# Kernel optimization log

Hardware: AMD Instinct MI355X
Metric: run time of the kernel (lower is better)

The kernel has to match this reference:

```python
import jax, jax.numpy as jnp
import numpy as np

B, D, L = 8, 512, 4096
NHEAD = 8
HEAD_DIM = D // NHEAD
TRUNC_STD = 0.02


def setup_inputs() -> dict:
    key = jax.random.key(0)
    ks = jax.random.split(key, 7)
    return {
        "x": jax.random.normal(ks[0], (B, D, L, 1), jnp.float32),
        "y": jax.random.normal(ks[1], (B, D, 1, 1), jnp.float32),
        "Wq": jax.random.normal(ks[2], (D, D), jnp.float32) * TRUNC_STD,
        "Wk": jax.random.normal(ks[3], (D, D), jnp.float32) * TRUNC_STD,
        "Wv": jax.random.normal(ks[4], (D, D), jnp.float32) * TRUNC_STD,
        "WO_ring": jax.random.normal(ks[5], (D, D), jnp.float32) * TRUNC_STD,
        "bO_ring": jnp.zeros((D,), jnp.float32),
        "WO_star": jax.random.normal(ks[6], (D, D), jnp.float32) * TRUNC_STD,
        "bO_star": jnp.zeros((D,), jnp.float32),
    }


def reference(x, y, Wq, Wk, Wv, WO_ring, bO_ring, WO_star, bO_star):
    Bx, Dx, Lx, _ = x.shape
    hd = Dx // NHEAD
    scale = 1.0 / np.sqrt(hd).astype(np.float32)

    # concat relay token on the sequence axis, project q/k/v over channels
    xy = jnp.concatenate([x, y], axis=2)[..., 0]            # [B, D, L+1]
    xy = jnp.transpose(xy, (0, 2, 1))                       # [B, L+1, D]
    q = jnp.transpose(xy @ Wq, (0, 2, 1))                   # [B, D, L+1]
    k = jnp.transpose(xy @ Wk, (0, 2, 1))
    v = jnp.transpose(xy @ Wv, (0, 2, 1))

    # ---- ring (local window-3 + relay) attention over the L node tokens ----
    qn = q[:, :, :Lx].reshape(Bx, NHEAD, hd, Lx)            # [B,n,h,L]
    kn, vn = k[:, :, :Lx], v[:, :, :Lx]                     # [B,D,L]
    kr, vr = k[:, :, Lx], v[:, :, Lx]                       # [B,D]

    def window3(t):
        # extract_patches SAME with size 3: slot w holds t[:, :, l-1+w], zero-padded
        tp = jnp.pad(t, ((0, 0), (0, 0), (1, 1)))
        tw = jnp.stack([tp[:, :, w:w + Lx] for w in range(3)], axis=2)  # [B,D,3,L]
        return tw.reshape(Bx, NHEAD, hd, 3, Lx)

    kr_b = jnp.broadcast_to(kr.reshape(Bx, NHEAD, hd, 1, 1), (Bx, NHEAD, hd, 1, Lx))
    vr_b = jnp.broadcast_to(vr.reshape(Bx, NHEAD, hd, 1, 1), (Bx, NHEAD, hd, 1, Lx))
    kw = jnp.concatenate([window3(kn), kr_b], axis=3)       # [B,n,h,4,L]
    vw = jnp.concatenate([window3(vn), vr_b], axis=3)

    scores = jnp.einsum('bnhl,bnhwl->bnwl', qn, kw) * scale  # [B,n,4,L]
    alphas = jax.nn.softmax(scores, axis=2)                  # softmax over window
    att = jnp.einsum('bnwl,bnhwl->bnhl', alphas, vw).reshape(Bx, Dx, Lx)
    nodes = jnp.einsum('bdl,de->bel', att, WO_ring) + bO_ring[None, :, None]
    nodes = nodes[..., None]                                 # [B, D, L, 1]

    # ---- star (relay) attention: relay query attends to all L+1 tokens ----
    qr = q[:, :, Lx].reshape(Bx, NHEAD, 1, hd)              # [B,n,1,h]
    ka = k.reshape(Bx, NHEAD, hd, Lx + 1)                   # [B,n,h,L+1]
    va = v.reshape(Bx, NHEAD, hd, Lx + 1)
    s = jnp.einsum('bnoh,bnhl->bnol', qr, ka) * scale       # [B,n,1,L+1]
    a = jax.nn.softmax(s, axis=-1)
    att_r = jnp.einsum('bnol,bnhl->bnoh', a, va).reshape(Bx, Dx)
    relay = (att_r @ WO_star + bO_star).reshape(Bx, Dx, 1, 1)

    return nodes, relay
```

## Files before the change

kernel.cpp:

```cpp
#include <hip/hip_runtime.h>

#define BB 8
#define DD 512
#define LL 4096
#define NH 8
#define HD 64
#define SCALE 0.125f
#define NCH 16
#define CH 256

typedef __attribute__((ext_vector_type(8))) short short8;
typedef __attribute__((ext_vector_type(4))) float f32x4;

static __device__ __forceinline__ float bf2f(unsigned short u) {
  union { float f; unsigned int i; } c; c.i = ((unsigned int)u) << 16; return c.f;
}
static __device__ __forceinline__ unsigned short f2bf(float f) {
  union { float f; unsigned int i; } c; c.f = f;
  unsigned int i = c.i;
  unsigned int r = (i + 0x7fffu + ((i >> 16) & 1u)) >> 16;
  return (unsigned short)r;
}

static __device__ __forceinline__ void gload_lds16(const void* g, void* l) {
  __builtin_amdgcn_global_load_lds(
      (const __attribute__((address_space(1))) void*)g,
      (__attribute__((address_space(3))) void*)l, 16, 0, 0);
}

static __device__ __forceinline__ float waveSum(float v) {
#pragma unroll
  for (int o = 32; o; o >>= 1) v += __shfl_down(v, o, 64);
  return v;
}
static __device__ __forceinline__ float waveMax(float v) {
#pragma unroll
  for (int o = 32; o; o >>= 1) v = fmaxf(v, __shfl_down(v, o, 64));
  return v;
}
static __device__ __forceinline__ float grp8Sum(float v) {
  v += __shfl_xor(v, 1, 8);
  v += __shfl_xor(v, 2, 8);
  v += __shfl_xor(v, 4, 8);
  return v;
}
static __device__ float blockSum(float v, float* red) {
  const int lane = threadIdx.x & 63, wid = threadIdx.x >> 6;
  const int nw = (int)(blockDim.x >> 6);
  v = waveSum(v);
  if (lane == 0) red[wid] = v;
  __syncthreads();
  if (wid == 0) {
    float t = (lane < nw) ? red[lane] : 0.f;
    t = waveSum(t);
    if (lane == 0) red[0] = t;
  }
  __syncthreads();
  float r = red[0];
  __syncthreads();
  return r;
}
static __device__ float blockMax(float v, float* red) {
  const int lane = threadIdx.x & 63, wid = threadIdx.x >> 6;
  const int nw = (int)(blockDim.x >> 6);
  v = waveMax(v);
  if (lane == 0) red[wid] = v;
  __syncthreads();
  if (wid == 0) {
    float t = (lane < nw) ? red[lane] : -1e30f;
    t = waveMax(t);
    if (lane == 0) red[0] = t;
  }
  __syncthreads();
  float r = red[0];
  __syncthreads();
  return r;
}

__global__ __launch_bounds__(256) void prep_w4(
    const float* __restrict__ w0, const float* __restrict__ w1,
    const float* __restrict__ w2, const float* __restrict__ w3,
    unsigned short* __restrict__ o0, unsigned short* __restrict__ o1,
    unsigned short* __restrict__ o2, unsigned short* __restrict__ o3) {
  const int s = blockIdx.z;
  const float* win = (s == 0) ? w0 : (s == 1) ? w1 : (s == 2) ? w2 : w3;
  unsigned short* wout = (s == 0) ? o0 : (s == 1) ? o1 : (s == 2) ? o2 : o3;
  const int d0 = blockIdx.y * 64;
  const int m0 = blockIdx.x * 64;
  __shared__ float t[64][65];
  const int tid = threadIdx.x;
  const int r = tid >> 4;
  const int c4 = (tid & 15) * 4;
#pragma unroll
  for (int p = 0; p < 4; p++) {
    const float4 v = *(const float4*)(win + (size_t)(d0 + p * 16 + r) * DD + m0 + c4);
    *(float4*)&t[p * 16 + r][c4] = v;
  }
  __syncthreads();
#pragma unroll
  for (int p = 0; p < 4; p++) {
    const int ll = p * 16 + r;
    ushort4 o;
    o.x = f2bf(t[c4 + 0][ll]);
    o.y = f2bf(t[c4 + 1][ll]);
    o.z = f2bf(t[c4 + 2][ll]);
    o.w = f2bf(t[c4 + 3][ll]);
    *(ushort4*)(wout + (size_t)(m0 + ll) * DD + d0 + c4) = o;
  }
}

__global__ __launch_bounds__(256) void prep_x(
    const float* __restrict__ x, unsigned short* __restrict__ xt) {
  const int b = blockIdx.z;
  const int e0 = blockIdx.y * 64;
  const int l0 = blockIdx.x * 64;
  __shared__ float t[64][65];
  const int tid = threadIdx.x;
  const int r = tid >> 4;
  const int c4 = (tid & 15) * 4;
  const float* xb = x + (size_t)b * DD * LL;
#pragma unroll
  for (int p = 0; p < 4; p++) {
    const float4 v = *(const float4*)(xb + (size_t)(e0 + p * 16 + r) * LL + l0 + c4);
    *(float4*)&t[p * 16 + r][c4] = v;
  }
  __syncthreads();
#pragma unroll
  for (int p = 0; p < 4; p++) {
    const int ll = p * 16 + r;
    ushort4 o;
    o.x = f2bf(t[c4 + 0][ll]);
    o.y = f2bf(t[c4 + 1][ll]);
    o.z = f2bf(t[c4 + 2][ll]);
    o.w = f2bf(t[c4 + 3][ll]);
    *(ushort4*)(xt + ((size_t)b * LL + l0 + ll) * DD + e0 + c4) = o;
  }
}

#define STAGEH(g, s)                                       \
  do {                                                     \
    gload_lds16((g) + sgoff, (s) + sloff);                 \
    gload_lds16((g) + sgoff + 32, (s) + sloff + 4096);     \
  } while (0)

#define READ_A(dst, base, ib)                                           \
  _Pragma("unroll") for (int i = 0; i < 4; i++) {                       \
    dst[i][0] = *(const short8*)((base) + ((ib) + i) * 512);            \
    dst[i][1] = *(const short8*)((base) + ((ib) + i) * 512 + 4096);     \
  }

#define READ_B(base, qn_)                                               \
  _Pragma("unroll") for (int j = 0; j < 2; j++) {                       \
    bb[j][0] = *(const short8*)((base) + (qn_) * 1024 + j * 512);       \
    bb[j][1] = *(const short8*)((base) + (qn_) * 1024 + j * 512 + 4096);\
  }

#define MFMA16(AF, IO, JO)                                                    \
  __builtin_amdgcn_s_setprio(1);                                              \
  _Pragma("unroll") for (int i = 0; i < 4; i++)                               \
  _Pragma("unroll") for (int j = 0; j < 2; j++) {                             \
    acc[(IO) + i][(JO) + j] = __builtin_amdgcn_mfma_f32_16x16x32_bf16(        \
        AF[i][0], bb[j][0], acc[(IO) + i][(JO) + j], 0, 0, 0);                \
    acc[(IO) + i][(JO) + j] = __builtin_amdgcn_mfma_f32_16x16x32_bf16(        \
        AF[i][1], bb[j][1], acc[(IO) + i][(JO) + j], 0, 0, 0);                \
  }                                                                           \
  __builtin_amdgcn_s_setprio(0);

#define PHASE_SYNC_PRE                                     \
  __builtin_amdgcn_s_barrier();                            \
  asm volatile("s_waitcnt lgkmcnt(0)" ::: "memory");       \
  __builtin_amdgcn_sched_barrier(0);

#define PHASE_SYNC_POST                                    \
  __builtin_amdgcn_sched_barrier(0);                       \
  __builtin_amdgcn_s_barrier();

__global__ __launch_bounds__(512, 2) void qkv_mfma_8ph(
    const unsigned short* __restrict__ Wt, const unsigned short* __restrict__ Xt,
    unsigned short* __restrict__ qn, unsigned short* __restrict__ kn,
    unsigned short* __restrict__ vn) {
  extern __shared__ __align__(16) unsigned short sm[];
  const int b = blockIdx.z;
  const int m0 = blockIdx.y * 256;
  const int n0 = blockIdx.x * 256;
  const int tid = threadIdx.x;
  const int lane = tid & 63, w = tid >> 6;
  const int wm = w >> 2, wn = w & 3;
  const int l15 = lane & 15, lh = lane >> 4;

  const unsigned short* Ag = Wt + (size_t)m0 * DD;
  const unsigned short* Bg = Xt + ((size_t)b * LL + n0) * DD;

  const int kswz = (lh << 3) ^ ((l15 & 8) << 1);
  const unsigned short* aB = sm + wm * 8192 + l15 * 32 + kswz;
  const unsigned short* bB = sm + 32768 + (wn >> 1) * 8192 + (wn & 1) * 2048 +
                             l15 * 32 + kswz;

  const int srow = (w << 4) + (lane >> 2);
  const size_t sgoff = (size_t)srow * DD + ((size_t)(((lane & 3) << 3) ^ ((srow & 8) << 1)));
  const int sloff = w * 512;

  f32x4 acc[8][4];
#pragma unroll
  for (int i = 0; i < 8; i++)
#pragma unroll
    for (int j = 0; j < 4; j++) acc[i][j] = (f32x4){0.f, 0.f, 0.f, 0.f};

  STAGEH(Ag, sm);
  STAGEH(Ag + 128 * DD, sm + 8192);
  STAGEH(Bg, sm + 32768);
  STAGEH(Bg + 128 * DD, sm + 32768 + 8192);
  STAGEH(Ag + 64, sm + 16384);
  STAGEH(Ag + 128 * DD + 64, sm + 16384 + 8192);
  asm volatile("s_waitcnt vmcnt(4)" ::: "memory");
  __builtin_amdgcn_s_barrier();

  short8 a0[4][2], a1[4][2], bb[2][2];
  for (int u = 0; u < 8; ++u) {
    const int slot = u & 1;
    const unsigned short* aS = aB + slot * 16384;
    const unsigned short* bS = bB + slot * 16384;
    const unsigned short* An = Ag + (u + 2) * 64;
    const unsigned short* Bn = Bg + (u + 1) * 64;
    unsigned short* sAd = sm + slot * 16384;
    unsigned short* sBd = sm + 32768 + (slot ^ 1) * 16384;

    READ_A(a0, aS, 0);
    READ_B(bS, 0);
    if (u < 7) STAGEH(Bn, sBd);
    PHASE_SYNC_PRE
    MFMA16(a0, 0, 0)
    PHASE_SYNC_POST
    READ_A(a1, aS, 4);
    if (u < 7) STAGEH(Bn + 128 * DD, sBd + 8192);
    PHASE_SYNC_PRE
    MFMA16(a1, 4, 0)
    PHASE_SYNC_POST
    READ_B(bS, 1);
    if (u < 6) STAGEH(An, sAd);
    PHASE_SYNC_PRE
    MFMA16(a0, 0, 2)
    PHASE_SYNC_POST
    if (u < 6) STAGEH(An + 128 * DD, sAd + 8192);
    __builtin_amdgcn_s_barrier();
    asm volatile("s_waitcnt lgkmcnt(0)" ::: "memory");
    __builtin_amdgcn_sched_barrier(0);
    MFMA16(a1, 4, 2)
    __builtin_amdgcn_sched_barrier(0);
    if (u < 6) {
      asm volatile("s_waitcnt vmcnt(4)" ::: "memory");
    } else if (u == 6) {
      asm volatile("s_waitcnt vmcnt(0)" ::: "memory");
    }
    __builtin_amdgcn_s_barrier();
  }

  __syncthreads();
#pragma unroll
  for (int i = 0; i < 8; i++)
#pragma unroll
    for (int j = 0; j < 4; j++) {
      const int dloc = wm * 128 + i * 16 + lh * 4;
      const int lloc = wn * 64 + j * 16 + l15;
      ushort4 pk;
      pk.x = f2bf(acc[i][j][0]);
      pk.y = f2bf(acc[i][j][1]);
      pk.z = f2bf(acc[i][j][2]);
      pk.w = f2bf(acc[i][j][3]);
      *(ushort4*)((char*)sm + ((lloc * 512 + dloc * 2) ^ ((lloc & 7) << 4))) = pk;
    }
  __syncthreads();
  const int sector = m0 >> 9;
  unsigned short* outp = ((sector == 0) ? qn : (sector == 1) ? kn : vn) +
                         (size_t)b * LL * DD + (m0 & 511);
#pragma unroll
  for (int it = 0; it < 16; it++) {
    const int flat = it * 8192 + tid * 16;
    const int lloc = flat >> 9;
    const int off = flat & 511;
    const short8 vdat =
        *(const short8*)((const char*)sm + lloc * 512 + (off ^ ((lloc & 7) << 4)));
    *(short8*)(outp + (size_t)(n0 + lloc) * DD + (off >> 1)) = vdat;
  }
}

__global__ __launch_bounds__(256) void nodes_mfma(
    const unsigned short* __restrict__ Wt, const unsigned short* __restrict__ At,
    const float* __restrict__ bo, float* __restrict__ out) {
  const int wgid = blockIdx.x + 32 * (blockIdx.y + 4 * blockIdx.z);
  const int swz = (wgid & 7) * 128 + (wgid >> 3);
  const int b = swz >> 7;
  const int rem = swz & 127;
  const int n0 = (rem >> 2) * 128;
  const int m0 = (rem & 3) * 128;
  __shared__ short As[128 * 32];
  __shared__ short Bs[128 * 32];
  const int tid = threadIdx.x;
  const int lane = tid & 63, w = tid >> 6;
  const int wm = w & 1, wn = w >> 1;

  const unsigned short* Ag = Wt + (size_t)m0 * DD;
  const unsigned short* Bg = At + ((size_t)b * LL + n0) * DD;
  const int srow = lane >> 2;
  const int scol = (lane & 3) * 8;

  f32x4 acc[4][4];
#pragma unroll
  for (int i = 0; i < 4; i++)
#pragma unroll
    for (int j = 0; j < 4; j++) acc[i][j] = (f32x4){0.f, 0.f, 0.f, 0.f};

  for (int k0 = 0; k0 < DD; k0 += 32) {
    __syncthreads();
#pragma unroll
    for (int p = 0; p < 2; p++) {
      const int c = w * 2 + p;
      gload_lds16(Ag + (size_t)(c * 16 + srow) * DD + k0 + scol, (short*)As + c * 16 * 32);
      gload_lds16(Bg + (size_t)(c * 16 + srow) * DD + k0 + scol, (short*)Bs + c * 16 * 32);
    }
    __syncthreads();
    short8 af[4], bfr[4];
#pragma unroll
    for (int i = 0; i < 4; i++)
      af[i] = *(const short8*)&As[(wm * 64 + i * 16 + (lane & 15)) * 32 + (lane >> 4) * 8];
#pragma unroll
    for (int j = 0; j < 4; j++)
      bfr[j] = *(const short8*)&Bs[(wn * 64 + j * 16 + (lane & 15)) * 32 + (lane >> 4) * 8];
#pragma unroll
    for (int i = 0; i < 4; i++)
#pragma unroll
      for (int j = 0; j < 4; j++)
        acc[i][j] = __builtin_amdgcn_mfma_f32_16x16x32_bf16(af[i], bfr[j], acc[i][j], 0, 0, 0);
  }

  float* outp = out + (size_t)b * DD * LL;
  const int ebase = m0 + wm * 64;
  const int col0 = n0 + wn * 64 + (lane & 15);
#pragma unroll
  for (int i = 0; i < 4; i++) {
    const int e0 = ebase + i * 16 + (lane >> 4) * 4;
#pragma unroll
    for (int j = 0; j < 4; j++) {
      const int cc = col0 + j * 16;
#pragma unroll
      for (int r = 0; r < 4; r++)
        outp[(size_t)(e0 + r) * LL + cc] = acc[i][j][r] + bo[e0 + r];
    }
  }
}

__global__ __launch_bounds__(256) void relay_qkv(
    const float* __restrict__ y, const float* __restrict__ Wq,
    const float* __restrict__ Wk, const float* __restrict__ Wv,
    float* __restrict__ qr, float* __restrict__ kr, float* __restrict__ vr) {
  const int b = blockIdx.y;
  const int d = blockIdx.x * 256 + threadIdx.x;
  __shared__ float ys[DD];
  for (int i = threadIdx.x; i < DD; i += 256) ys[i] = y[b * DD + i];
  __syncthreads();
  float aq = 0.f, ak = 0.f, av = 0.f;
  for (int e = 0; e < DD; e++) {
    const float yv = ys[e];
    aq = fmaf(yv, Wq[(size_t)e * DD + d], aq);
    ak = fmaf(yv, Wk[(size_t)e * DD + d], ak);
    av = fmaf(yv, Wv[(size_t)e * DD + d], av);
  }
  qr[b * DD + d] = aq;
  kr[b * DD + d] = ak;
  vr[b * DD + d] = av;
}

__global__ __launch_bounds__(256) void local_attn(
    const unsigned short* __restrict__ qn, const unsigned short* __restrict__ kn,
    const unsigned short* __restrict__ vn, const float* __restrict__ kr,
    const float* __restrict__ vr, unsigned short* __restrict__ att_t) {
  const int b = blockIdx.z, n = blockIdx.y;
  const int tid = threadIdx.x;
  const int li = tid >> 3, dl = tid & 7;
  const int l0 = blockIdx.x * 32;
  const int l = l0 + li;
  __shared__ float krs[HD], vrs[HD];
  __shared__ __align__(16) char ksb[34 * 128];
  __shared__ __align__(16) char vsb[34 * 128];
  const int rb = b * DD + n * HD;
  if (tid < HD) { krs[tid] = kr[rb + tid]; vrs[tid] = vr[rb + tid]; }

  {
    const int s1 = tid >> 3;
    const int gl1 = min(max(l0 - 1 + s1, 0), LL - 1);
    const size_t gb1 = ((size_t)b * LL + gl1) * DD + n * HD + dl * 8;
    const int so1 = s1 * 128 + dl * 16;
    *(short8*)(ksb + so1) = *(const short8*)(kn + gb1);
    *(short8*)(vsb + so1) = *(const short8*)(vn + gb1);
    if (tid < 16) {
      const int s2 = 32 + (tid >> 3);
      const int gl2 = min(l0 - 1 + s2, LL - 1);
      const size_t gb2 = ((size_t)b * LL + gl2) * DD + n * HD + dl * 8;
      const int so2 = s2 * 128 + dl * 16;
      *(short8*)(ksb + so2) = *(const short8*)(kn + gb2);
      *(short8*)(vsb + so2) = *(const short8*)(vn + gb2);
    }
  }
  __syncthreads();

  const size_t rowbase = ((size_t)b * LL + l) * DD + n * HD + dl * 8;
  const bool has_m = (l > 0), has_p = (l < LL - 1);
  const int lo = dl * 16;

  const short8 q8 = *(const short8*)(qn + rowbase);
  const short8 km8 = *(const short8*)(ksb + (li + 0) * 128 + lo);
  const short8 k08 = *(const short8*)(ksb + (li + 1) * 128 + lo);
  const short8 kp8 = *(const short8*)(ksb + (li + 2) * 128 + lo);

  float s0 = 0.f, s1 = 0.f, s2 = 0.f, s3 = 0.f;
  float qf[8];
#pragma unroll
  for (int j = 0; j < 8; j++) {
    qf[j] = bf2f((unsigned short)q8[j]);
    s0 = fmaf(qf[j], bf2f((unsigned short)km8[j]), s0);
    s1 = fmaf(qf[j], bf2f((unsigned short)k08[j]), s1);
    s2 = fmaf(qf[j], bf2f((unsigned short)kp8[j]), s2);
    s3 = fmaf(qf[j], krs[dl * 8 + j], s3);
  }
  s0 = grp8Sum(s0) * SCALE;
  s1 = grp8Sum(s1) * SCALE;
  s2 = grp8Sum(s2) * SCALE;
  s3 = grp8Sum(s3) * SCALE;
  if (!has_m) s0 = 0.f;
  if (!has_p) s2 = 0.f;
  const float m = fmaxf(fmaxf(s0, s1), fmaxf(s2, s3));
  const float e0 = __expf(s0 - m), e1 = __expf(s1 - m);
  const float e2 = __expf(s2 - m), e3 = __expf(s3 - m);
  const float inv = 1.f / (e0 + e1 + e2 + e3);
  const float a0 = has_m ? e0 * inv : 0.f;
  const float a1 = e1 * inv;
  const float a2 = has_p ? e2 * inv : 0.f;
  const float a3 = e3 * inv;

  const short8 vm8 = *(const short8*)(vsb + (li + 0) * 128 + lo);
  const short8 v08 = *(const short8*)(vsb + (li + 1) * 128 + lo);
  const short8 vp8 = *(const short8*)(vsb + (li + 2) * 128 + lo);
  short8 o8;
#pragma unroll
  for (int j = 0; j < 8; j++) {
    float o = a0 * bf2f((unsigned short)vm8[j]) + a1 * bf2f((unsigned short)v08[j]) +
              a2 * bf2f((unsigned short)vp8[j]) + a3 * vrs[dl * 8 + j];
    o8[j] = (short)f2bf(o);
  }
  *(short8*)(att_t + rowbase) = o8;
}

__global__ __launch_bounds__(256) void relay_attn_part(
    const float* __restrict__ qr, const unsigned short* __restrict__ kn,
    const unsigned short* __restrict__ vn, float* __restrict__ part) {
  const int ch = blockIdx.x, n = blockIdx.y, b = blockIdx.z;
  const int tid = threadIdx.x;
  const int li = tid >> 3, dl = tid & 7;
  __shared__ float qs[HD];
  __shared__ float sv[CH];
  __shared__ float red[17];
  __shared__ float os[32][68];
  const int rb = b * DD + n * HD;
  if (tid < HD) qs[tid] = qr[rb + tid];
  __syncthreads();
  const size_t base = ((size_t)b * LL + ch * CH) * DD + n * HD + dl * 8;

#pragma unroll
  for (int it = 0; it < 8; it++) {
    const int lr2 = it * 32 + li;
    const short8 kc = *(const short8*)(kn + base + (size_t)lr2 * DD);
    float p = 0.f;
#pragma unroll
    for (int j = 0; j < 8; j++) p = fmaf(qs[dl * 8 + j], bf2f((unsigned short)kc[j]), p);
    p = grp8Sum(p);
    if (dl == 0) sv[lr2] = p * SCALE;
  }
  __syncthreads();
  const float s = sv[tid];
  const float m = blockMax(s, red);
  const float pp = __expf(s - m);
  sv[tid] = pp;
  const float sum = blockSum(pp, red);

  float oc[8];
#pragma unroll
  for (int j = 0; j < 8; j++) oc[j] = 0.f;
#pragma unroll
  for (int it = 0; it < 8; it++) {
    const int lr2 = it * 32 + li;
    const float p = sv[lr2];
    const short8 vc = *(const short8*)(vn + base + (size_t)lr2 * DD);
#pragma unroll
    for (int j = 0; j < 8; j++) oc[j] = fmaf(p, bf2f((unsigned short)vc[j]), oc[j]);
  }
#pragma unroll
  for (int j = 0; j < 8; j++) os[li][dl * 8 + j] = oc[j];
  __syncthreads();
  float* po = part + (((size_t)b * NH + n) * NCH + ch) * 68;
  if (tid < HD) {
    float t = 0.f;
#pragma unroll 8
    for (int g = 0; g < 32; g++) t += os[g][tid];
    po[tid] = t;
  }
  if (tid == 64) { po[64] = m; po[65] = sum; }
}

__global__ __launch_bounds__(64) void relay_attn_combine(
    const float* __restrict__ qr, const float* __restrict__ krr,
    const float* __restrict__ vrr, const float* __restrict__ part,
    float* __restrict__ attr) {
  const int n = blockIdx.x, b = blockIdx.y;
  const int h = threadIdx.x;
  const int rb = b * DD + n * HD;
  float t = qr[rb + h] * krr[rb + h];
  t = waveSum(t);
  const float s_r = __shfl(t, 0, 64) * SCALE;
  const float* po = part + (((size_t)b * NH + n) * NCH) * 68;
  float M = s_r;
#pragma unroll
  for (int c = 0; c < NCH; c++) M = fmaxf(M, po[c * 68 + 64]);
  float S = __expf(s_r - M);
  float o = S * vrr[rb + h];
#pragma unroll
  for (int c = 0; c < NCH; c++) {
    const float e = __expf(po[c * 68 + 64] - M);
    S = fmaf(po[c * 68 + 65], e, S);
    o = fmaf(po[c * 68 + h], e, o);
  }
  attr[rb + h] = o / S;
}

__global__ __launch_bounds__(256) void relay_proj(
    const float* __restrict__ attr, const float* __restrict__ Wstar,
    const float* __restrict__ bstar, float* __restrict__ out) {
  const int b = blockIdx.y;
  const int e = blockIdx.x * 256 + threadIdx.x;
  __shared__ float as[DD];
  for (int i = threadIdx.x; i < DD; i += 256) as[i] = attr[b * DD + i];
  __syncthreads();
  float acc = bstar[e];
  for (int d = 0; d < DD; d++) acc = fmaf(as[d], Wstar[(size_t)d * DD + e], acc);
  out[(size_t)BB * DD * LL + b * DD + e] = acc;
}

extern "C" void kernel_launch(void* const* d_in, const int* in_sizes, int n_in,
                              void* d_out, int out_size, void* d_ws, size_t ws_size,
                              hipStream_t stream) {
  const float* x   = (const float*)d_in[0];
  const float* y   = (const float*)d_in[1];
  const float* Wq  = (const float*)d_in[2];
  const float* Wk  = (const float*)d_in[3];
  const float* Wv  = (const float*)d_in[4];
  const float* WOr = (const float*)d_in[5];
  const float* bOr = (const float*)d_in[6];
  const float* WOs = (const float*)d_in[7];
  const float* bOs = (const float*)d_in[8];
  float* out = (float*)d_out;

  char* ws = (char*)d_ws;
  const size_t SZ = (size_t)BB * DD * LL * sizeof(unsigned short);
  unsigned short* qn  = (unsigned short*)(ws);
  unsigned short* kn  = (unsigned short*)(ws + SZ);
  unsigned short* vn  = (unsigned short*)(ws + 2 * SZ);
  unsigned short* xt  = (unsigned short*)(ws + 3 * SZ);
  unsigned short* att_t = xt;
  unsigned short* Wallt = (unsigned short*)(ws + 4 * SZ);
  unsigned short* WOrt  = (unsigned short*)(ws + 4 * SZ + 1536 * 512 * 2);
  float* qr   = (float*)(ws + 4 * SZ + 2048 * 512 * 2);
  float* kr   = qr + BB * DD;
  float* vr   = kr + BB * DD;
  float* attr = vr + BB * DD;
  float* part = attr + BB * DD;

  static int smaxset = 0;
  if (!smaxset) {
    (void)hipFuncSetAttribute((const void*)qkv_mfma_8ph,
                              hipFuncAttributeMaxDynamicSharedMemorySize, 131072);
    smaxset = 1;
  }

  prep_w4<<<dim3(8, 8, 4), 256, 0, stream>>>(
      Wq, Wk, Wv, WOr,
      Wallt, Wallt + (size_t)512 * 512, Wallt + (size_t)1024 * 512, WOrt);
  prep_x<<<dim3(64, 8, BB), 256, 0, stream>>>(x, xt);

  qkv_mfma_8ph<<<dim3(16, 6, BB), 512, 131072, stream>>>(Wallt, xt, qn, kn, vn);
  relay_qkv<<<dim3(DD / 256, BB), 256, 0, stream>>>(y, Wq, Wk, Wv, qr, kr, vr);
  local_attn<<<dim3(LL / 32, NH, BB), 256, 0, stream>>>(qn, kn, vn, kr, vr, att_t);
  nodes_mfma<<<dim3(32, 4, BB), 256, 0, stream>>>(WOrt, att_t, bOr, out);
  relay_attn_part<<<dim3(NCH, NH, BB), 256, 0, stream>>>(qr, kn, vn, part);
  relay_attn_combine<<<dim3(NH, BB), 64, 0, stream>>>(qr, kr, vr, part, attr);
  relay_proj<<<dim3(DD / 256, BB), 256, 0, stream>>>(attr, WOs, bOs, out);
}
```

Before: 307.3 us.

## Fuse relay attention partials into local attention and split-K relay matvecs

Computes the star-attention partial softmax and weighted sum per 32-token tile inside the local attention kernel, reusing the K/V rows already staged in shared memory. This removes the separate relay_attn_part kernel and its second full read of kn/vn. The combine step now merges 128 chunks instead of 16. The relay q/k/v and output-projection matvecs are split across four warps along the reduction dimension, giving more blocks, with a shared-memory final sum.

```diff
diff --git a/kernel.cpp b/kernel.cpp
--- a/kernel.cpp
+++ b/kernel.cpp
@@ -6,8 +6,7 @@
 #define NH 8
 #define HD 64
 #define SCALE 0.125f
-#define NCH 16
-#define CH 256
+#define NCH2 128
 
 typedef __attribute__((ext_vector_type(8))) short short8;
 typedef __attribute__((ext_vector_type(4))) float f32x4;
@@ -33,48 +32,21 @@
   for (int o = 32; o; o >>= 1) v += __shfl_down(v, o, 64);
   return v;
 }
-static __device__ __forceinline__ float waveMax(float v) {
-#pragma unroll
-  for (int o = 32; o; o >>= 1) v = fmaxf(v, __shfl_down(v, o, 64));
-  return v;
-}
 static __device__ __forceinline__ float grp8Sum(float v) {
   v += __shfl_xor(v, 1, 8);
   v += __shfl_xor(v, 2, 8);
   v += __shfl_xor(v, 4, 8);
   return v;
 }
-static __device__ float blockSum(float v, float* red) {
-  const int lane = threadIdx.x & 63, wid = threadIdx.x >> 6;
-  const int nw = (int)(blockDim.x >> 6);
-  v = waveSum(v);
-  if (lane == 0) red[wid] = v;
-  __syncthreads();
-  if (wid == 0) {
-    float t = (lane < nw) ? red[lane] : 0.f;
-    t = waveSum(t);
-    if (lane == 0) red[0] = t;
-  }
-  __syncthreads();
-  float r = red[0];
-  __syncthreads();
-  return r;
-}
-static __device__ float blockMax(float v, float* red) {
-  const int lane = threadIdx.x & 63, wid = threadIdx.x >> 6;
-  const int nw = (int)(blockDim.x >> 6);
-  v = waveMax(v);
-  if (lane == 0) red[wid] = v;
-  __syncthreads();
-  if (wid == 0) {
-    float t = (lane < nw) ? red[lane] : -1e30f;
-    t = waveMax(t);
-    if (lane == 0) red[0] = t;
-  }
-  __syncthreads();
-  float r = red[0];
-  __syncthreads();
-  return r;
+static __device__ __forceinline__ float waveAllMax(float v) {
+#pragma unroll
+  for (int o = 1; o < 64; o <<= 1) v = fmaxf(v, __shfl_xor(v, o, 64));
+  return v;
+}
+static __device__ __forceinline__ float waveAllSum(float v) {
+#pragma unroll
+  for (int o = 1; o < 64; o <<= 1) v += __shfl_xor(v, o, 64);
+  return v;
 }
 
 __global__ __launch_bounds__(256) void prep_w4(
@@ -354,36 +326,54 @@
     const float* __restrict__ Wk, const float* __restrict__ Wv,
     float* __restrict__ qr, float* __restrict__ kr, float* __restrict__ vr) {
   const int b = blockIdx.y;
-  const int d = blockIdx.x * 256 + threadIdx.x;
+  const int d0 = blockIdx.x * 64;
+  const int tid = threadIdx.x;
+  const int dl = tid & 63, eg = tid >> 6;
   __shared__ float ys[DD];
-  for (int i = threadIdx.x; i < DD; i += 256) ys[i] = y[b * DD + i];
+  __shared__ float r3[3][4][64];
+  for (int i = tid; i < DD; i += 256) ys[i] = y[b * DD + i];
   __syncthreads();
   float aq = 0.f, ak = 0.f, av = 0.f;
-  for (int e = 0; e < DD; e++) {
+  const int e0 = eg * 128;
+  for (int e = e0; e < e0 + 128; e++) {
     const float yv = ys[e];
-    aq = fmaf(yv, Wq[(size_t)e * DD + d], aq);
-    ak = fmaf(yv, Wk[(size_t)e * DD + d], ak);
-    av = fmaf(yv, Wv[(size_t)e * DD + d], av);
-  }
-  qr[b * DD + d] = aq;
-  kr[b * DD + d] = ak;
-  vr[b * DD + d] = av;
-}
-
-__global__ __launch_bounds__(256) void local_attn(
+    aq = fmaf(yv, Wq[(size_t)e * DD + d0 + dl], aq);
+    ak = fmaf(yv, Wk[(size_t)e * DD + d0 + dl], ak);
+    av = fmaf(yv, Wv[(size_t)e * DD + d0 + dl], av);
+  }
+  r3[0][eg][dl] = aq;
+  r3[1][eg][dl] = ak;
+  r3[2][eg][dl] = av;
+  __syncthreads();
+  if (tid < 192) {
+    const int m = tid >> 6, d = tid & 63;
+    const float s = r3[m][0][d] + r3[m][1][d] + r3[m][2][d] + r3[m][3][d];
+    float* dst = (m == 0) ? qr : (m == 1) ? kr : vr;
+    dst[b * DD + d0 + d] = s;
+  }
+}
+
+__global__ __launch_bounds__(256) void local_attn_f(
     const unsigned short* __restrict__ qn, const unsigned short* __restrict__ kn,
     const unsigned short* __restrict__ vn, const float* __restrict__ kr,
-    const float* __restrict__ vr, unsigned short* __restrict__ att_t) {
+    const float* __restrict__ vr, const float* __restrict__ qrg,
+    unsigned short* __restrict__ att_t, float* __restrict__ part) {
   const int b = blockIdx.z, n = blockIdx.y;
   const int tid = threadIdx.x;
   const int li = tid >> 3, dl = tid & 7;
   const int l0 = blockIdx.x * 32;
   const int l = l0 + li;
-  __shared__ float krs[HD], vrs[HD];
+  __shared__ float krs[HD], vrs[HD], qrs[HD];
   __shared__ __align__(16) char ksb[34 * 128];
   __shared__ __align__(16) char vsb[34 * 128];
+  __shared__ float sv2[32];
+  __shared__ float os[32][68];
   const int rb = b * DD + n * HD;
-  if (tid < HD) { krs[tid] = kr[rb + tid]; vrs[tid] = vr[rb + tid]; }
+  if (tid < HD) {
+    krs[tid] = kr[rb + tid];
+    vrs[tid] = vr[rb + tid];
+    qrs[tid] = qrg[rb + tid];
+  }
 
   {
     const int s1 = tid >> 3;
@@ -448,62 +438,35 @@
     o8[j] = (short)f2bf(o);
   }
   *(short8*)(att_t + rowbase) = o8;
-}
-
-__global__ __launch_bounds__(256) void relay_attn_part(
-    const float* __restrict__ qr, const unsigned short* __restrict__ kn,
-    const unsigned short* __restrict__ vn, float* __restrict__ part) {
-  const int ch = blockIdx.x, n = blockIdx.y, b = blockIdx.z;
-  const int tid = threadIdx.x;
-  const int li = tid >> 3, dl = tid & 7;
-  __shared__ float qs[HD];
-  __shared__ float sv[CH];
-  __shared__ float red[17];
-  __shared__ float os[32][68];
-  const int rb = b * DD + n * HD;
-  if (tid < HD) qs[tid] = qr[rb + tid];
-  __syncthreads();
-  const size_t base = ((size_t)b * LL + ch * CH) * DD + n * HD + dl * 8;
-
-#pragma unroll
-  for (int it = 0; it < 8; it++) {
-    const int lr2 = it * 32 + li;
-    const short8 kc = *(const short8*)(kn + base + (size_t)lr2 * DD);
+
+  {
+    const short8 kc = *(const short8*)(ksb + (li + 1) * 128 + lo);
     float p = 0.f;
 #pragma unroll
-    for (int j = 0; j < 8; j++) p = fmaf(qs[dl * 8 + j], bf2f((unsigned short)kc[j]), p);
+    for (int j = 0; j < 8; j++) p = fmaf(qrs[dl * 8 + j], bf2f((unsigned short)kc[j]), p);
     p = grp8Sum(p);
-    if (dl == 0) sv[lr2] = p * SCALE;
-  }
-  __syncthreads();
-  const float s = sv[tid];
-  const float m = blockMax(s, red);
-  const float pp = __expf(s - m);
-  sv[tid] = pp;
-  const float sum = blockSum(pp, red);
-
-  float oc[8];
-#pragma unroll
-  for (int j = 0; j < 8; j++) oc[j] = 0.f;
-#pragma unroll
-  for (int it = 0; it < 8; it++) {
-    const int lr2 = it * 32 + li;
-    const float p = sv[lr2];
-    const short8 vc = *(const short8*)(vn + base + (size_t)lr2 * DD);
-#pragma unroll
-    for (int j = 0; j < 8; j++) oc[j] = fmaf(p, bf2f((unsigned short)vc[j]), oc[j]);
-  }
-#pragma unroll
-  for (int j = 0; j < 8; j++) os[li][dl * 8 + j] = oc[j];
-  __syncthreads();
-  float* po = part + (((size_t)b * NH + n) * NCH + ch) * 68;
+    if (dl == 0) sv2[li] = p * SCALE;
+  }
+  __syncthreads();
+  const int lane = tid & 63;
+  const float sval = sv2[lane & 31];
+  const float m2 = waveAllMax(sval);
+  const float sum2 = waveAllSum((lane < 32) ? __expf(sval - m2) : 0.f);
+  const float pp = __expf(sv2[li] - m2);
+  {
+    const short8 vc = *(const short8*)(vsb + (li + 1) * 128 + lo);
+#pragma unroll
+    for (int j = 0; j < 8; j++) os[li][dl * 8 + j] = pp * bf2f((unsigned short)vc[j]);
+  }
+  __syncthreads();
+  float* po = part + (((size_t)b * NH + n) * NCH2 + blockIdx.x) * 68;
   if (tid < HD) {
     float t = 0.f;
 #pragma unroll 8
     for (int g = 0; g < 32; g++) t += os[g][tid];
     po[tid] = t;
   }
-  if (tid == 64) { po[64] = m; po[65] = sum; }
+  if (tid == 64) { po[64] = m2; po[65] = sum2; }
 }
 
 __global__ __launch_bounds__(64) void relay_attn_combine(
@@ -516,14 +479,14 @@
   float t = qr[rb + h] * krr[rb + h];
   t = waveSum(t);
   const float s_r = __shfl(t, 0, 64) * SCALE;
-  const float* po = part + (((size_t)b * NH + n) * NCH) * 68;
+  const float* po = part + (((size_t)b * NH + n) * NCH2) * 68;
   float M = s_r;
-#pragma unroll
-  for (int c = 0; c < NCH; c++) M = fmaxf(M, po[c * 68 + 64]);
+#pragma unroll 8
+  for (int c = 0; c < NCH2; c++) M = fmaxf(M, po[c * 68 + 64]);
   float S = __expf(s_r - M);
   float o = S * vrr[rb + h];
-#pragma unroll
-  for (int c = 0; c < NCH; c++) {
+#pragma unroll 4
+  for (int c = 0; c < NCH2; c++) {
     const float e = __expf(po[c * 68 + 64] - M);
     S = fmaf(po[c * 68 + 65], e, S);
     o = fmaf(po[c * 68 + h], e, o);
@@ -535,13 +498,22 @@
     const float* __restrict__ attr, const float* __restrict__ Wstar,
     const float* __restrict__ bstar, float* __restrict__ out) {
   const int b = blockIdx.y;
-  const int e = blockIdx.x * 256 + threadIdx.x;
+  const int e0 = blockIdx.x * 64;
+  const int tid = threadIdx.x;
+  const int el = tid & 63, dg = tid >> 6;
   __shared__ float as[DD];
-  for (int i = threadIdx.x; i < DD; i += 256) as[i] = attr[b * DD + i];
-  __syncthreads();
-  float acc = bstar[e];
-  for (int d = 0; d < DD; d++) acc = fmaf(as[d], Wstar[(size_t)d * DD + e], acc);
-  out[(size_t)BB * DD * LL + b * DD + e] = acc;
+  __shared__ float r[4][64];
+  for (int i = tid; i < DD; i += 256) as[i] = attr[b * DD + i];
+  __syncthreads();
+  float acc = 0.f;
+  const int d0 = dg * 128;
+  for (int d = d0; d < d0 + 128; d++)
+    acc = fmaf(as[d], Wstar[(size_t)d * DD + e0 + el], acc);
+  r[dg][el] = acc;
+  __syncthreads();
+  if (tid < 64)
+    out[(size_t)BB * DD * LL + b * DD + e0 + tid] =
+        r[0][tid] + r[1][tid] + r[2][tid] + r[3][tid] + bstar[e0 + tid];
 }
 
 extern "C" void kernel_launch(void* const* d_in, const int* in_sizes, int n_in,
@@ -586,10 +558,10 @@
   prep_x<<<dim3(64, 8, BB), 256, 0, stream>>>(x, xt);
 
   qkv_mfma_8ph<<<dim3(16, 6, BB), 512, 131072, stream>>>(Wallt, xt, qn, kn, vn);
-  relay_qkv<<<dim3(DD / 256, BB), 256, 0, stream>>>(y, Wq, Wk, Wv, qr, kr, vr);
-  local_attn<<<dim3(LL / 32, NH, BB), 256, 0, stream>>>(qn, kn, vn, kr, vr, att_t);
+  relay_qkv<<<dim3(8, BB), 256, 0, stream>>>(y, Wq, Wk, Wv, qr, kr, vr);
+  local_attn_f<<<dim3(LL / 32, NH, BB), 256, 0, stream>>>(qn, kn, vn, kr, vr, qr,
+                                                          att_t, part);
   nodes_mfma<<<dim3(32, 4, BB), 256, 0, stream>>>(WOrt, att_t, bOr, out);
-  relay_attn_part<<<dim3(NCH, NH, BB), 256, 0, stream>>>(qr, kn, vn, part);
   relay_attn_combine<<<dim3(NH, BB), 64, 0, stream>>>(qr, kr, vr, part, attr);
-  relay_proj<<<dim3(DD / 256, BB), 256, 0, stream>>>(attr, WOs, bOs, out);
-}
+  relay_proj<<<dim3(8, BB), 256, 0, stream>>>(attr, WOs, bOs, out);
+}
```

New measurement: 294.9 us. 4.0% less time.
